# Optimization experiments

Hardware: AMD Instinct MI355X
Metric: run time of the kernel (lower is better)

Reference implementation:

```python
import jax, jax.numpy as jnp
import numpy as np

B, S, D, H = 2, 2048, 1024, 16
AD = D // H  # per-head dim = 64


def setup_inputs() -> dict:
    key = jax.random.key(0)
    k1, k2, k3 = jax.random.split(key, 3)
    x = jax.random.normal(k1, (B, S, D), dtype=jnp.float32)
    W_qkv = jax.random.normal(k2, (D, 3 * D), dtype=jnp.float32) * (1.0 / np.sqrt(D))
    b_qkv = jax.random.normal(k3, (3 * D,), dtype=jnp.float32) * 0.01
    return {"x": x, "W_qkv": W_qkv, "b_qkv": b_qkv}


def reference(x, W_qkv, b_qkv):
    b, s, _ = x.shape
    qkv = x @ W_qkv + b_qkv                      # [B,S,3D]
    qkv = qkv.reshape(b, s, H, 3 * AD)           # per-head interleaved qkv
    qkv = jnp.transpose(qkv, (0, 2, 1, 3))       # [B,H,S,3*ad]
    q = qkv[..., :AD]
    k = qkv[..., AD:2 * AD]
    v = qkv[..., 2 * AD:]
    scale = 1.0 / jnp.sqrt(jnp.asarray(AD, dtype=x.dtype))
    att = jnp.einsum("bhqd,bhkd->bhqk", q, k) * scale  # [B,H,S,S]
    att = jax.nn.softmax(att, axis=-1)
    values = jnp.einsum("bhqk,bhkd->bhqd", att, v)     # [B,H,S,ad]
    # Faithful to source: reshape [B,H,S,ad] -> [B,S,ad*H] WITHOUT head transpose
    return values.reshape(b, s, AD * H)
```

## Files before the change

### kernel.cpp

```cpp
#include <hip/hip_runtime.h>
#include <stdint.h>
#include <stddef.h>

#define S_LEN 2048
#define NH 16
#define HD 64
#define DM 1024
#define NQKV 3072
#define MROWS 4096
#define NBH 32

typedef float f32x4 __attribute__((ext_vector_type(4)));
typedef __bf16 bf16x8 __attribute__((ext_vector_type(8)));
typedef __bf16 bf16x4 __attribute__((ext_vector_type(4)));
typedef __bf16 bf16x2v __attribute__((ext_vector_type(2)));
typedef short short8_t __attribute__((ext_vector_type(8)));
typedef unsigned int u32x4 __attribute__((ext_vector_type(4)));

__device__ __forceinline__ unsigned short f2bf(float f) {
  union { float f; unsigned int u; } v; v.f = f;
  unsigned int u = v.u;
  u += 0x7FFFu + ((u >> 16) & 1u);
  return (unsigned short)(u >> 16);
}

__device__ __forceinline__ float exp2_raw(float x) {
  return __builtin_amdgcn_exp2f(x);
}

__device__ __forceinline__ void async_copy16(const void* g, void* l) {
  __builtin_amdgcn_global_load_lds(
      (const __attribute__((address_space(1))) void*)g,
      (__attribute__((address_space(3))) void*)l, 16, 0, 0);
}

#define WAITCNT_BARRIER(N)                                          \
  asm volatile("s_waitcnt vmcnt(" #N ")" ::: "memory");             \
  __builtin_amdgcn_sched_barrier(0);                                \
  __builtin_amdgcn_s_barrier();                                     \
  __builtin_amdgcn_sched_barrier(0);

__global__ __launch_bounds__(256) void prep_kernel(const float* __restrict__ x,
                                                   unsigned short* __restrict__ xb,
                                                   const float* __restrict__ W,
                                                   unsigned short* __restrict__ wt) {
  if (blockIdx.x < 2048) {
    size_t i = ((size_t)blockIdx.x * 256 + threadIdx.x) * 8;
    f32x4 a = *(const f32x4*)(x + i);
    f32x4 b = *(const f32x4*)(x + i + 4);
    union { unsigned short u[8]; short8_t v; } o;
    o.u[0] = f2bf(a[0]); o.u[1] = f2bf(a[1]); o.u[2] = f2bf(a[2]); o.u[3] = f2bf(a[3]);
    o.u[4] = f2bf(b[0]); o.u[5] = f2bf(b[1]); o.u[6] = f2bf(b[2]); o.u[7] = f2bf(b[3]);
    *(short8_t*)(xb + i) = o.v;
  } else {
    __shared__ float tile[32][33];
    const int wb = blockIdx.x - 2048;
    const int n0 = (wb % 96) * 32;
    const int k0 = (wb / 96) * 32;
    const int tx = threadIdx.x & 31;
    const int ty = threadIdx.x >> 5;
    #pragma unroll
    for (int i = 0; i < 4; ++i)
      tile[ty + i * 8][tx] = W[(size_t)(k0 + ty + i * 8) * NQKV + n0 + tx];
    __syncthreads();
    #pragma unroll
    for (int i = 0; i < 4; ++i)
      wt[(size_t)(n0 + ty + i * 8) * DM + k0 + tx] = f2bf(tile[tx][ty + i * 8]);
  }
}

__global__ __launch_bounds__(256) void qkv_gemm_kernel(
    const unsigned short* __restrict__ xb, const unsigned short* __restrict__ wt,
    const float* __restrict__ bias,
    unsigned short* __restrict__ Qb, unsigned short* __restrict__ Kb,
    unsigned short* __restrict__ Vt) {
  __shared__ __align__(16) unsigned char Sh[4][128 * 64 * 2];
  const int t = threadIdx.x;
  const int lane = t & 63;
  const int wave = t >> 6;
  const int wm = (wave >> 1) * 64, wn = (wave & 1) * 64;
  const int lr = lane & 15, g = lane >> 4;
  const int m0 = blockIdx.x * 128, n0 = blockIdx.y * 128;

  f32x4 acc[4][4];
  #pragma unroll
  for (int i = 0; i < 4; ++i)
    #pragma unroll
    for (int j = 0; j < 4; ++j) acc[i][j] = f32x4{0.f, 0.f, 0.f, 0.f};

  auto stage = [&](int kt, int buf) __attribute__((always_inline)) {
    const int k0 = kt * 64;
    #pragma unroll
    for (int i = 0; i < 4; ++i) {
      int c = t + i * 256;
      int row = c >> 3;
      int cc = (c & 7) ^ (row & 7);
      async_copy16(xb + (size_t)(m0 + row) * DM + k0 + cc * 8, Sh[buf * 2] + c * 16);
      async_copy16(wt + (size_t)(n0 + row) * DM + k0 + cc * 8, Sh[buf * 2 + 1] + c * 16);
    }
  };

  auto compute = [&](int buf) __attribute__((always_inline)) {
    unsigned char* const As = Sh[buf * 2];
    unsigned char* const Bs = Sh[buf * 2 + 1];
    bf16x8 af[2][4], bfr[2][4];
    #pragma unroll
    for (int kk = 0; kk < 2; ++kk) {
      #pragma unroll
      for (int i = 0; i < 4; ++i) {
        int ra = wm + i * 16 + lr;
        af[kk][i] = *(const bf16x8*)(As + ((ra * 128 + kk * 64 + g * 16) ^ ((ra & 7) << 4)));
        int rb = wn + i * 16 + lr;
        bfr[kk][i] = *(const bf16x8*)(Bs + ((rb * 128 + kk * 64 + g * 16) ^ ((rb & 7) << 4)));
      }
    }
    __builtin_amdgcn_s_setprio(1);
    #pragma unroll
    for (int kk = 0; kk < 2; ++kk)
      #pragma unroll
      for (int mi = 0; mi < 4; ++mi)
        #pragma unroll
        for (int ni = 0; ni < 4; ++ni)
          acc[mi][ni] = __builtin_amdgcn_mfma_f32_16x16x32_bf16(
              af[kk][mi], bfr[kk][ni], acc[mi][ni], 0, 0, 0);
    __builtin_amdgcn_s_setprio(0);
  };

  stage(0, 0);
  __syncthreads();
  for (int kt = 0; kt < DM / 64; kt += 2) {
    stage(kt + 1, 1);
    compute(0);
    __syncthreads();
    if (kt + 2 < DM / 64) stage(kt + 2, 0);
    compute(1);
    __syncthreads();
  }

  const float QSC = 0.18033688011112042f;
  const int nbase = n0 + wn;
  const int h = nbase / 192;
  const int typ = (nbase % 192) >> 6;
  const int b = m0 >> 11;
  const int bh = b * NH + h;

  if (typ == 2) {
    unsigned char* const T = Sh[0] + wave * 8192;
    #pragma unroll
    for (int ni = 0; ni < 4; ++ni) {
      int col = ni * 16 + lr;
      float bv = bias[nbase + col];
      #pragma unroll
      for (int mi = 0; mi < 4; ++mi) {
        bf16x4 w;
        w[0] = (__bf16)(acc[mi][ni][0] + bv);
        w[1] = (__bf16)(acc[mi][ni][1] + bv);
        w[2] = (__bf16)(acc[mi][ni][2] + bv);
        w[3] = (__bf16)(acc[mi][ni][3] + bv);
        int byte = (col * 128 + (mi * 16 + g * 4) * 2) ^ ((col & 7) << 4);
        *(bf16x4*)(T + byte) = w;
      }
    }
    asm volatile("s_waitcnt lgkmcnt(0)" ::: "memory");
    __builtin_amdgcn_sched_barrier(0);
    const int s0 = (m0 & 2047) + wm + (lane & 7) * 8;
    #pragma unroll
    for (int i = 0; i < 8; ++i) {
      int col = i * 8 + (lane >> 3);
      int byte = (col * 128 + (lane & 7) * 16) ^ ((col & 7) << 4);
      bf16x8 v = *(const bf16x8*)(T + byte);
      *(bf16x8*)(Vt + ((size_t)bh * HD + col) * S_LEN + s0) = v;
    }
  } else {
    unsigned short* const dst = (typ == 0) ? Qb : Kb;
    const float sc = (typ == 0) ? QSC : 1.0f;
    #pragma unroll
    for (int ni = 0; ni < 4; ++ni) {
      int d = ni * 16 + lr;
      float bv = bias[nbase + d];
      #pragma unroll
      for (int mi = 0; mi < 4; ++mi) {
        #pragma unroll
        for (int r = 0; r < 4; ++r) {
          int s = (m0 & 2047) + wm + mi * 16 + g * 4 + r;
          dst[((size_t)bh * S_LEN + s) * HD + d] = f2bf((acc[mi][ni][r] + bv) * sc);
        }
      }
    }
  }
}

__global__ __launch_bounds__(512) void attn_kernel(
    const unsigned short* __restrict__ Qb, const unsigned short* __restrict__ Kb,
    const unsigned short* __restrict__ Vt, float* __restrict__ out) {
  __shared__ __align__(16) unsigned char smem[65536];
  const int t = threadIdx.x;
  const int lane = t & 63;
  const int wave = t >> 6;
  const int lr = lane & 15, g = lane >> 4;
  const int bh = blockIdx.y;
  const int q0 = blockIdx.x * 128 + wave * 16;

  const unsigned short* Qbh = Qb + (size_t)bh * S_LEN * HD;
  const unsigned short* Kbh = Kb + (size_t)bh * S_LEN * HD;
  const unsigned short* Vbh = Vt + (size_t)bh * HD * S_LEN;

  bf16x8 qf[2];
  #pragma unroll
  for (int kk = 0; kk < 2; ++kk)
    qf[kk] = *(const bf16x8*)(Qbh + (size_t)(q0 + lr) * HD + kk * 32 + g * 8);

  union { unsigned short u[8]; bf16x8 v; } one_c;
  #pragma unroll
  for (int j = 0; j < 8; ++j) one_c.u[j] = 0x3F80;
  const bf16x8 ones8 = one_c.v;

  const f32x4 ZERO = f32x4{0.f, 0.f, 0.f, 0.f};

  int kvOff[4][2];
  #pragma unroll
  for (int i = 0; i < 4; ++i)
    #pragma unroll
    for (int kk = 0; kk < 2; ++kk) {
      int r = i * 16 + lr;
      kvOff[i][kk] = (r * 128 + kk * 64 + g * 16) ^ ((r & 7) << 4);
    }

  const int c0 = t;
  const int row0 = c0 >> 3;
  const int cc0 = (c0 & 7) ^ (row0 & 7);
  const int kGO0 = row0 * HD + cc0 * 8;
  const int vGO0 = row0 * S_LEN + cc0 * 8;

  f32x4 lacc = f32x4{0.f, 0.f, 0.f, 0.f};
  f32x4 oacc[4];
  #pragma unroll
  for (int di = 0; di < 4; ++di) oacc[di] = f32x4{0.f, 0.f, 0.f, 0.f};

  auto stage = [&](int kt, int buf) __attribute__((always_inline)) {
    const unsigned short* kp = Kbh + (size_t)kt * (64 * HD);
    const unsigned short* vp = Vbh + kt * 64;
    unsigned char* const base = smem + buf * 16384;
    async_copy16(kp + kGO0, base + c0 * 16);
    async_copy16(vp + vGO0, base + 8192 + c0 * 16);
  };

  auto compute = [&](int buf) __attribute__((always_inline)) {
    unsigned char* const Ksb = smem + buf * 16384;
    unsigned char* const Vsb = Ksb + 8192;
    f32x4 sacc[4];
    __builtin_amdgcn_s_setprio(1);
    #pragma unroll
    for (int ni = 0; ni < 4; ++ni) {
      bf16x8 kf0 = *(const bf16x8*)(Ksb + kvOff[ni][0]);
      sacc[ni] = __builtin_amdgcn_mfma_f32_16x16x32_bf16(kf0, qf[0], ZERO, 0, 0, 0);
      bf16x8 kf1 = *(const bf16x8*)(Ksb + kvOff[ni][1]);
      sacc[ni] = __builtin_amdgcn_mfma_f32_16x16x32_bf16(kf1, qf[1], sacc[ni], 0, 0, 0);
    }
    __builtin_amdgcn_s_setprio(0);

    unsigned wv[4][2];
    #pragma unroll
    for (int ni = 0; ni < 4; ++ni) {
      bf16x2v w0;
      w0[0] = (__bf16)exp2_raw(sacc[ni][0]);
      w0[1] = (__bf16)exp2_raw(sacc[ni][1]);
      wv[ni][0] = __builtin_bit_cast(unsigned, w0);
      bf16x2v w1;
      w1[0] = (__bf16)exp2_raw(sacc[ni][2]);
      w1[1] = (__bf16)exp2_raw(sacc[ni][3]);
      wv[ni][1] = __builtin_bit_cast(unsigned, w1);
    }

    bf16x8 pf[2];
    #pragma unroll
    for (int kk = 0; kk < 2; ++kk) {
      unsigned A = wv[2 * kk][0], B = wv[2 * kk][1];
      unsigned C = wv[2 * kk + 1][0], D = wv[2 * kk + 1][1];
      asm("v_permlane32_swap_b32 %0, %1" : "+v"(A), "+v"(C));
      asm("v_permlane32_swap_b32 %0, %1" : "+v"(B), "+v"(D));
      asm("v_permlane16_swap_b32 %0, %1" : "+v"(A), "+v"(C));
      asm("v_permlane16_swap_b32 %0, %1" : "+v"(B), "+v"(D));
      u32x4 tmp; tmp[0] = A; tmp[1] = B; tmp[2] = C; tmp[3] = D;
      pf[kk] = __builtin_bit_cast(bf16x8, tmp);
    }

    __builtin_amdgcn_s_setprio(1);
    #pragma unroll
    for (int di = 0; di < 4; ++di)
      #pragma unroll
      for (int kk = 0; kk < 2; ++kk) {
        bf16x8 vf = *(const bf16x8*)(Vsb + kvOff[di][kk]);
        oacc[di] = __builtin_amdgcn_mfma_f32_16x16x32_bf16(vf, pf[kk], oacc[di], 0, 0, 0);
      }
    #pragma unroll
    for (int kk = 0; kk < 2; ++kk)
      lacc = __builtin_amdgcn_mfma_f32_16x16x32_bf16(ones8, pf[kk], lacc, 0, 0, 0);
    __builtin_amdgcn_s_setprio(0);
  };

  stage(0, 0);
  stage(1, 1);
  for (int kt4 = 0; kt4 < 28; kt4 += 4) {
    stage(kt4 + 2, 2); WAITCNT_BARRIER(4); compute(0);
    stage(kt4 + 3, 3); WAITCNT_BARRIER(4); compute(1);
    stage(kt4 + 4, 0); WAITCNT_BARRIER(4); compute(2);
    stage(kt4 + 5, 1); WAITCNT_BARRIER(4); compute(3);
  }
  stage(30, 2); WAITCNT_BARRIER(4); compute(0);
  stage(31, 3); WAITCNT_BARRIER(4); compute(1);
  WAITCNT_BARRIER(2); compute(2);
  WAITCNT_BARRIER(0); compute(3);

  float inv = 1.0f / lacc[0];
  float* outp = out + ((size_t)bh * S_LEN + q0 + lr) * HD;
  #pragma unroll
  for (int di = 0; di < 4; ++di) {
    f32x4 o = oacc[di] * inv;
    *(f32x4*)(outp + di * 16 + g * 4) = o;
  }
}

extern "C" void kernel_launch(void* const* d_in, const int* in_sizes, int n_in,
                              void* d_out, int out_size, void* d_ws, size_t ws_size,
                              hipStream_t stream) {
  const float* x    = (const float*)d_in[0];
  const float* W    = (const float*)d_in[1];
  const float* bias = (const float*)d_in[2];
  float* out = (float*)d_out;

  unsigned short* xb = (unsigned short*)d_ws;
  unsigned short* wt = xb + (size_t)MROWS * DM;
  unsigned short* Qb = wt + (size_t)NQKV * DM;
  unsigned short* Kb = Qb + (size_t)NBH * S_LEN * HD;
  unsigned short* Vt = Kb + (size_t)NBH * S_LEN * HD;

  prep_kernel<<<2048 + 3072, 256, 0, stream>>>(x, xb, W, wt);
  qkv_gemm_kernel<<<dim3(MROWS / 128, NQKV / 128), 256, 0, stream>>>(xb, wt, bias, Qb, Kb, Vt);
  attn_kernel<<<dim3(S_LEN / 128, NBH), 512, 0, stream>>>(Qb, Kb, Vt, out);
}
```

Before: 82.42 us.

## Use 128-key tiles with double buffering and block-wide syncs in attention

The attention loop now stages 128-key K/V tiles instead of 64-key tiles, with each thread issuing four async copies per stage. It replaces the four-buffer ring, which used per-stage vmcnt waits and barriers, with two buffers and __syncthreads. Each 128-key tile is processed as two 64-key halves, and V gets its own 16-chunk XOR swizzle. This halves the number of barriers and loop iterations, but gives up the deeper prefetch distance and the partial waits, so load latency may be exposed more.

```diff
diff --git a/kernel.cpp b/kernel.cpp
--- a/kernel.cpp
+++ b/kernel.cpp
@@ -33,12 +33,6 @@
       (const __attribute__((address_space(1))) void*)g,
       (__attribute__((address_space(3))) void*)l, 16, 0, 0);
 }
-
-#define WAITCNT_BARRIER(N)                                          \
-  asm volatile("s_waitcnt vmcnt(" #N ")" ::: "memory");             \
-  __builtin_amdgcn_sched_barrier(0);                                \
-  __builtin_amdgcn_s_barrier();                                     \
-  __builtin_amdgcn_sched_barrier(0);
 
 __global__ __launch_bounds__(256) void prep_kernel(const float* __restrict__ x,
                                                    unsigned short* __restrict__ xb,
@@ -217,20 +211,30 @@
 
   const f32x4 ZERO = f32x4{0.f, 0.f, 0.f, 0.f};
 
-  int kvOff[4][2];
+  int kOff[4][2];
   #pragma unroll
   for (int i = 0; i < 4; ++i)
     #pragma unroll
     for (int kk = 0; kk < 2; ++kk) {
       int r = i * 16 + lr;
-      kvOff[i][kk] = (r * 128 + kk * 64 + g * 16) ^ ((r & 7) << 4);
-    }
-
-  const int c0 = t;
-  const int row0 = c0 >> 3;
-  const int cc0 = (c0 & 7) ^ (row0 & 7);
-  const int kGO0 = row0 * HD + cc0 * 8;
-  const int vGO0 = row0 * S_LEN + cc0 * 8;
+      kOff[i][kk] = (r * 128 + kk * 64 + g * 16) ^ ((r & 7) << 4);
+    }
+  int vOff[4][4];
+  #pragma unroll
+  for (int di = 0; di < 4; ++di)
+    #pragma unroll
+    for (int c2 = 0; c2 < 4; ++c2) {
+      int rv = di * 16 + lr;
+      vOff[di][c2] = rv * 256 + ((c2 * 64 + g * 16) ^ ((rv & 15) << 4));
+    }
+
+  const int cA = t, cB = t + 512;
+  const int krA = cA >> 3, krB = cB >> 3;
+  const int kcA = (cA & 7) ^ (krA & 7), kcB = (cB & 7) ^ (krB & 7);
+  const int kGOA = krA * HD + kcA * 8, kGOB = krB * HD + kcB * 8;
+  const int vrA = cA >> 4, vrB = cB >> 4;
+  const int vcA = (cA & 15) ^ (vrA & 15), vcB = (cB & 15) ^ (vrB & 15);
+  const int vGOA = vrA * S_LEN + vcA * 8, vGOB = vrB * S_LEN + vcB * 8;
 
   f32x4 lacc = f32x4{0.f, 0.f, 0.f, 0.f};
   f32x4 oacc[4];
@@ -238,23 +242,25 @@
   for (int di = 0; di < 4; ++di) oacc[di] = f32x4{0.f, 0.f, 0.f, 0.f};
 
   auto stage = [&](int kt, int buf) __attribute__((always_inline)) {
-    const unsigned short* kp = Kbh + (size_t)kt * (64 * HD);
-    const unsigned short* vp = Vbh + kt * 64;
-    unsigned char* const base = smem + buf * 16384;
-    async_copy16(kp + kGO0, base + c0 * 16);
-    async_copy16(vp + vGO0, base + 8192 + c0 * 16);
+    const unsigned short* kp = Kbh + (size_t)kt * (128 * HD);
+    const unsigned short* vp = Vbh + kt * 128;
+    unsigned char* const base = smem + buf * 32768;
+    async_copy16(kp + kGOA, base + cA * 16);
+    async_copy16(kp + kGOB, base + cB * 16);
+    async_copy16(vp + vGOA, base + 16384 + cA * 16);
+    async_copy16(vp + vGOB, base + 16384 + cB * 16);
   };
 
-  auto compute = [&](int buf) __attribute__((always_inline)) {
-    unsigned char* const Ksb = smem + buf * 16384;
-    unsigned char* const Vsb = Ksb + 8192;
+  auto compute = [&](int buf, int half) __attribute__((always_inline)) {
+    unsigned char* const Ksb = smem + buf * 32768 + half * 8192;
+    unsigned char* const Vsb = smem + buf * 32768 + 16384;
     f32x4 sacc[4];
     __builtin_amdgcn_s_setprio(1);
     #pragma unroll
     for (int ni = 0; ni < 4; ++ni) {
-      bf16x8 kf0 = *(const bf16x8*)(Ksb + kvOff[ni][0]);
+      bf16x8 kf0 = *(const bf16x8*)(Ksb + kOff[ni][0]);
       sacc[ni] = __builtin_amdgcn_mfma_f32_16x16x32_bf16(kf0, qf[0], ZERO, 0, 0, 0);
-      bf16x8 kf1 = *(const bf16x8*)(Ksb + kvOff[ni][1]);
+      bf16x8 kf1 = *(const bf16x8*)(Ksb + kOff[ni][1]);
       sacc[ni] = __builtin_amdgcn_mfma_f32_16x16x32_bf16(kf1, qf[1], sacc[ni], 0, 0, 0);
     }
     __builtin_amdgcn_s_setprio(0);
@@ -290,7 +296,7 @@
     for (int di = 0; di < 4; ++di)
       #pragma unroll
       for (int kk = 0; kk < 2; ++kk) {
-        bf16x8 vf = *(const bf16x8*)(Vsb + kvOff[di][kk]);
+        bf16x8 vf = *(const bf16x8*)(Vsb + vOff[di][half * 2 + kk]);
         oacc[di] = __builtin_amdgcn_mfma_f32_16x16x32_bf16(vf, pf[kk], oacc[di], 0, 0, 0);
       }
     #pragma unroll
@@ -300,17 +306,15 @@
   };
 
   stage(0, 0);
-  stage(1, 1);
-  for (int kt4 = 0; kt4 < 28; kt4 += 4) {
-    stage(kt4 + 2, 2); WAITCNT_BARRIER(4); compute(0);
-    stage(kt4 + 3, 3); WAITCNT_BARRIER(4); compute(1);
-    stage(kt4 + 4, 0); WAITCNT_BARRIER(4); compute(2);
-    stage(kt4 + 5, 1); WAITCNT_BARRIER(4); compute(3);
-  }
-  stage(30, 2); WAITCNT_BARRIER(4); compute(0);
-  stage(31, 3); WAITCNT_BARRIER(4); compute(1);
-  WAITCNT_BARRIER(2); compute(2);
-  WAITCNT_BARRIER(0); compute(3);
+  __syncthreads();
+  for (int kt = 0; kt < 16; kt += 2) {
+    stage(kt + 1, 1);
+    compute(0, 0); compute(0, 1);
+    __syncthreads();
+    if (kt + 2 < 16) stage(kt + 2, 0);
+    compute(1, 0); compute(1, 1);
+    __syncthreads();
+  }
 
   float inv = 1.0f / lacc[0];
   float* outp = out + ((size_t)bh * S_LEN + q0 + lr) * HD;
```

New measurement: 83.13 us. No clear change (+0.9%).
